# Performance work log

Measured on AMD Instinct MI355X. Metric: run time of the kernel, lower is better.

## Reference

```python
import jax, jax.numpy as jnp
import numpy as np

B, T = 64, 2000
Q_DIM, MEM_DIM, ATT_DIM = 1024, 512, 128
N_FILTERS, KERNEL = 32, 31


def setup_inputs() -> dict:
    key = jax.random.key(0)
    ks = jax.random.split(key, 8)
    s = lambda fan_in: 1.0 / np.sqrt(fan_in)
    return {
        "attention_hidden_state": jax.random.normal(ks[0], (B, Q_DIM), jnp.float32),
        "memory": jax.random.normal(ks[1], (B, T, MEM_DIM), jnp.float32),
        "attention_weights_cat": jax.random.uniform(ks[2], (B, 2, T), jnp.float32),
        "W_query": jax.random.normal(ks[3], (Q_DIM, ATT_DIM), jnp.float32) * s(Q_DIM),
        "W_memory": jax.random.normal(ks[4], (MEM_DIM, ATT_DIM), jnp.float32) * s(MEM_DIM),
        "W_v": jax.random.normal(ks[5], (ATT_DIM, 1), jnp.float32) * s(ATT_DIM),
        "W_conv": jax.random.normal(ks[6], (KERNEL, 2, N_FILTERS), jnp.float32) * s(KERNEL * 2),  # WIO layout
        "W_loc": jax.random.normal(ks[7], (N_FILTERS, ATT_DIM), jnp.float32) * s(N_FILTERS),
    }


def reference(attention_hidden_state, memory, attention_weights_cat,
              W_query, W_memory, W_v, W_conv, W_loc):
    # processed query: [B, 1, D]
    pq = jnp.tanh(attention_hidden_state @ W_query)[:, None, :]
    # processed memory: [B, T, D]
    pm = jnp.tanh(jnp.einsum('btm,md->btd', memory, W_memory))
    # location features: Conv1D 'same', no bias, channels-last input [B, T, 2]
    awc = jnp.transpose(attention_weights_cat, (0, 2, 1))
    conv = jax.lax.conv_general_dilated(
        awc, W_conv, window_strides=(1,), padding='SAME',
        dimension_numbers=('NWC', 'WIO', 'NWC'))  # [B, T, F]
    ploc = jnp.tanh(conv @ W_loc)  # [B, T, D]
    # energies: [B, T]
    energies = jnp.squeeze(jnp.tanh(pq + ploc + pm) @ W_v, -1)
    attention_weights = jax.nn.softmax(energies, axis=1)  # [B, T]
    attention_context = jnp.einsum('bt,btm->bm', attention_weights, memory)
    return attention_context, attention_weights
```

## Files before the change

kernel.cpp:

```cpp
#include <hip/hip_runtime.h>

typedef __attribute__((ext_vector_type(8))) short s16x8;
typedef __attribute__((ext_vector_type(4))) float f32x4;

#define B_SZ 64
#define T_SZ 2000
#define QD 1024
#define MD 512
#define AD 128
#define NF 32
#define KW 31
#define NTILE 63

__device__ __forceinline__ unsigned short f2bf(float f) {
    unsigned int u = __float_as_uint(f);
    unsigned int r = (u + 0x7FFFu + ((u >> 16) & 1u)) >> 16;
    return (unsigned short)r;
}
__device__ __forceinline__ unsigned int pack2bf(float a, float b) {
    return (unsigned int)f2bf(a) | ((unsigned int)f2bf(b) << 16);
}
__device__ __forceinline__ float fast_tanh(float x) {
    float ax = fabsf(x);
    float e = __expf(2.0f * ax);
    float r = 1.0f - 2.0f * __builtin_amdgcn_rcpf(e + 1.0f);
    return x < 0.0f ? -r : r;
}

__global__ __launch_bounds__(256) void prep_kernel(
    const float* __restrict__ ahs, const float* __restrict__ Wq,
    const float* __restrict__ Wm, const float* __restrict__ Wl,
    float* __restrict__ pq, unsigned short* __restrict__ WB,
    unsigned short* __restrict__ WL) {
    const int blk = blockIdx.x, tid = threadIdx.x;
    if (blk < 64) {
        __shared__ float q_sm[QD];
        ((float4*)q_sm)[tid] = ((const float4*)(ahs + blk * QD))[tid];
        __syncthreads();
        if (tid < AD) {
            float acc = 0.0f;
            for (int k = 0; k < QD; ++k) acc += q_sm[k] * Wq[k * AD + tid];
            pq[blk * AD + tid] = fast_tanh(acc);
        }
    } else if (blk < 96) {
        int cidx = (blk - 64) * 256 + tid;
        int n = cidx >> 10, s = (cidx >> 6) & 15, l = cidx & 63;
        int col = n * 16 + (l & 15);
        int krow = s * 32 + (l >> 4) * 8;
        float v[8];
        #pragma unroll
        for (int j = 0; j < 8; ++j) v[j] = Wm[(krow + j) * AD + col];
        uint4 pk;
        pk.x = pack2bf(v[0], v[1]); pk.y = pack2bf(v[2], v[3]);
        pk.z = pack2bf(v[4], v[5]); pk.w = pack2bf(v[6], v[7]);
        *(uint4*)(WB + cidx * 8) = pk;
    } else {
        for (int h = 0; h < 2; ++h) {
            int cidx = h * 256 + tid;
            int n = cidx >> 6, l = cidx & 63;
            int col = n * 16 + (l & 15);
            int krow = (l >> 4) * 8;
            float v[8];
            #pragma unroll
            for (int j = 0; j < 8; ++j) v[j] = Wl[(krow + j) * AD + col];
            uint4 pk;
            pk.x = pack2bf(v[0], v[1]); pk.y = pack2bf(v[2], v[3]);
            pk.z = pack2bf(v[4], v[5]); pk.w = pack2bf(v[6], v[7]);
            *(uint4*)(WL + cidx * 8) = pk;
        }
    }
}

__global__ __launch_bounds__(256) void energy_kernel(
    const float* __restrict__ memory, const float* __restrict__ awcat,
    const float* __restrict__ Wconv, const float* __restrict__ Wv,
    const float* __restrict__ pq, const unsigned short* __restrict__ WB,
    const unsigned short* __restrict__ WL, float* __restrict__ energies,
    float* __restrict__ ctile, float* __restrict__ mloc, int do_fuse) {
    const int tile = blockIdx.x;
    const int b = blockIdx.y;
    const int t0 = tile * 32;
    const int tid = threadIdx.x;

    __shared__ __align__(16) unsigned short Atile[32 * 512];
    __shared__ float aw_sm[2][64];
    __shared__ __align__(16) unsigned short conv_sm[32 * 40];
    __shared__ float e_part[32][4];
    __shared__ float p_sm[32];

    if (tid < 128) {
        int c = tid >> 6, i = tid & 63;
        float v = 0.0f;
        int tv = t0 - 15 + i;
        if (i < 63 && tv >= 0 && tv < T_SZ) v = awcat[(b * 2 + c) * T_SZ + tv];
        aw_sm[c][i] = v;
    }

    {
        const float4* msrc = (const float4*)(memory + ((size_t)b * T_SZ + t0) * MD);
        #pragma unroll
        for (int it = 0; it < 8; ++it) {
            int cid = it * 256 + tid;
            int r = cid >> 6, cc = cid & 63;
            float4 v0 = {0, 0, 0, 0}, v1 = {0, 0, 0, 0};
            if (t0 + r < T_SZ) {
                v0 = msrc[r * 128 + cc * 2];
                v1 = msrc[r * 128 + cc * 2 + 1];
            }
            uint4 pk;
            pk.x = pack2bf(v0.x, v0.y); pk.y = pack2bf(v0.z, v0.w);
            pk.z = pack2bf(v1.x, v1.y); pk.w = pack2bf(v1.z, v1.w);
            int off = (r * 1024 + cc * 16) ^ ((r & 7) << 4);
            *(uint4*)((char*)Atile + off) = pk;
        }
    }
    __syncthreads();

    {
        int f = tid & 31, tq = tid >> 5;
        float acc[4] = {0, 0, 0, 0};
        for (int k = 0; k < KW; ++k) {
            #pragma unroll
            for (int c = 0; c < 2; ++c) {
                float wv = Wconv[(k * 2 + c) * NF + f];
                #pragma unroll
                for (int tt = 0; tt < 4; ++tt)
                    acc[tt] += wv * aw_sm[c][tq + tt * 8 + k];
            }
        }
        #pragma unroll
        for (int tt = 0; tt < 4; ++tt)
            conv_sm[(tq + tt * 8) * 40 + f] = f2bf(acc[tt]);
    }
    __syncthreads();

    const int w = tid >> 6, l = tid & 63;
    const int lr = l & 15, lg = l >> 4;
    const int d0 = (2 * w + 0) * 16 + lr;
    const int d1 = (2 * w + 1) * 16 + lr;
    const float pqv0 = pq[b * AD + d0], pqv1 = pq[b * AD + d1];
    const float wvv0 = Wv[d0], wvv1 = Wv[d1];

    f32x4 zero4 = {0, 0, 0, 0};
    f32x4 p00 = zero4, p01 = zero4, p10 = zero4, p11 = zero4;

    const s16x8* wbp = (const s16x8*)WB;
    const int swz = (lr & 7) << 4;
    const int abase0 = lr * 1024 + lg * 16;
    const int abase1 = (16 + lr) * 1024 + lg * 16;

    #pragma unroll
    for (int s = 0; s < 16; ++s) {
        s16x8 a0 = *(const s16x8*)((const char*)Atile + ((abase0 + s * 64) ^ swz));
        s16x8 a1 = *(const s16x8*)((const char*)Atile + ((abase1 + s * 64) ^ swz));
        s16x8 b0 = wbp[((2 * w + 0) * 16 + s) * 64 + l];
        s16x8 b1 = wbp[((2 * w + 1) * 16 + s) * 64 + l];
        p00 = __builtin_amdgcn_mfma_f32_16x16x32_bf16(a0, b0, p00, 0, 0, 0);
        p01 = __builtin_amdgcn_mfma_f32_16x16x32_bf16(a0, b1, p01, 0, 0, 0);
        p10 = __builtin_amdgcn_mfma_f32_16x16x32_bf16(a1, b0, p10, 0, 0, 0);
        p11 = __builtin_amdgcn_mfma_f32_16x16x32_bf16(a1, b1, p11, 0, 0, 0);
    }

    s16x8 la0 = *(const s16x8*)((const char*)conv_sm + (lr * 80 + lg * 16));
    s16x8 la1 = *(const s16x8*)((const char*)conv_sm + ((16 + lr) * 80 + lg * 16));
    const s16x8* wlp = (const s16x8*)WL;
    s16x8 lb0 = wlp[(2 * w + 0) * 64 + l];
    s16x8 lb1 = wlp[(2 * w + 1) * 64 + l];
    f32x4 q00 = __builtin_amdgcn_mfma_f32_16x16x32_bf16(la0, lb0, zero4, 0, 0, 0);
    f32x4 q01 = __builtin_amdgcn_mfma_f32_16x16x32_bf16(la0, lb1, zero4, 0, 0, 0);
    f32x4 q10 = __builtin_amdgcn_mfma_f32_16x16x32_bf16(la1, lb0, zero4, 0, 0, 0);
    f32x4 q11 = __builtin_amdgcn_mfma_f32_16x16x32_bf16(la1, lb1, zero4, 0, 0, 0);

    float vr[8];
    #pragma unroll
    for (int r = 0; r < 4; ++r) {
        vr[r]     = fast_tanh(pqv0 + fast_tanh(q00[r]) + fast_tanh(p00[r])) * wvv0
                  + fast_tanh(pqv1 + fast_tanh(q01[r]) + fast_tanh(p01[r])) * wvv1;
        vr[4 + r] = fast_tanh(pqv0 + fast_tanh(q10[r]) + fast_tanh(p10[r])) * wvv0
                  + fast_tanh(pqv1 + fast_tanh(q11[r]) + fast_tanh(p11[r])) * wvv1;
    }
    #pragma unroll
    for (int j = 0; j < 8; ++j) {
        float v = vr[j];
        v += __shfl_xor(v, 1);
        v += __shfl_xor(v, 2);
        v += __shfl_xor(v, 4);
        v += __shfl_xor(v, 8);
        if (lr == 0) e_part[(j >> 2) * 16 + lg * 4 + (j & 3)][w] = v;
    }
    __syncthreads();

    if (tid < 32) {
        int t = t0 + tid;
        bool valid = t < T_SZ;
        float e = (e_part[tid][0] + e_part[tid][1]) + (e_part[tid][2] + e_part[tid][3]);
        if (valid) energies[b * T_SZ + t] = e;
        if (do_fuse) {
            float m = valid ? e : -3.4e38f;
            m = fmaxf(m, __shfl_xor(m, 1));
            m = fmaxf(m, __shfl_xor(m, 2));
            m = fmaxf(m, __shfl_xor(m, 4));
            m = fmaxf(m, __shfl_xor(m, 8));
            m = fmaxf(m, __shfl_xor(m, 16));
            p_sm[tid] = valid ? __expf(e - m) : 0.0f;
            if (tid == 0) mloc[b * NTILE + tile] = m;
        }
    }
    if (!do_fuse) return;
    __syncthreads();

    {
        float c0 = 0.0f, c1 = 0.0f;
        const int boff = tid * 4;
        #pragma unroll
        for (int t = 0; t < 32; ++t) {
            float p = p_sm[t];
            unsigned int pk = *(const unsigned int*)(
                (const char*)Atile + ((t * 1024 + boff) ^ ((t & 7) << 4)));
            c0 += p * __uint_as_float(pk << 16);
            c1 += p * __uint_as_float(pk & 0xffff0000u);
        }
        float2 o; o.x = c0; o.y = c1;
        ((float2*)ctile)[((b * NTILE + tile) << 8) + tid] = o;
    }
}

__global__ __launch_bounds__(256) void softmax_kernel(
    const float* __restrict__ energies, float* __restrict__ wout,
    float* __restrict__ Mb, float* __restrict__ invZb) {
    const int b = blockIdx.x, tid = threadIdx.x;
    const int lane = tid & 63, wv = tid >> 6;
    __shared__ float red[8];
    float ev[8];
    float m = -3.4e38f;
    #pragma unroll
    for (int i = 0; i < 8; ++i) {
        int idx = tid + i * 256;
        ev[i] = (idx < T_SZ) ? energies[b * T_SZ + idx] : -3.4e38f;
        m = fmaxf(m, ev[i]);
    }
    m = fmaxf(m, __shfl_xor(m, 1));  m = fmaxf(m, __shfl_xor(m, 2));
    m = fmaxf(m, __shfl_xor(m, 4));  m = fmaxf(m, __shfl_xor(m, 8));
    m = fmaxf(m, __shfl_xor(m, 16)); m = fmaxf(m, __shfl_xor(m, 32));
    if (lane == 0) red[wv] = m;
    __syncthreads();
    m = fmaxf(fmaxf(red[0], red[1]), fmaxf(red[2], red[3]));
    float p[8];
    float s = 0.0f;
    #pragma unroll
    for (int i = 0; i < 8; ++i) {
        int idx = tid + i * 256;
        p[i] = (idx < T_SZ) ? __expf(ev[i] - m) : 0.0f;
        s += p[i];
    }
    s += __shfl_xor(s, 1);  s += __shfl_xor(s, 2);
    s += __shfl_xor(s, 4);  s += __shfl_xor(s, 8);
    s += __shfl_xor(s, 16); s += __shfl_xor(s, 32);
    if (lane == 0) red[4 + wv] = s;
    __syncthreads();
    float Z = (red[4] + red[5]) + (red[6] + red[7]);
    float inv = 1.0f / Z;
    if (tid == 0) { Mb[b] = m; invZb[b] = inv; }
    #pragma unroll
    for (int i = 0; i < 8; ++i) {
        int idx = tid + i * 256;
        if (idx < T_SZ) wout[b * T_SZ + idx] = p[i] * inv;
    }
}

__global__ __launch_bounds__(256) void ctx_reduce_fused_kernel(
    const float* __restrict__ ctile, const float* __restrict__ mloc,
    const float* __restrict__ Mb, const float* __restrict__ invZb,
    float* __restrict__ ctx) {
    const int b = blockIdx.x, tid = threadIdx.x;
    const float M = Mb[b], iZ = invZb[b];
    float2 acc = {0.0f, 0.0f};
    #pragma unroll 7
    for (int tl = 0; tl < NTILE; ++tl) {
        float sc = __expf(mloc[b * NTILE + tl] - M);
        float2 v = ((const float2*)ctile)[((b * NTILE + tl) << 8) + tid];
        acc.x += sc * v.x;
        acc.y += sc * v.y;
    }
    float2 o; o.x = acc.x * iZ; o.y = acc.y * iZ;
    ((float2*)ctx)[(b << 8) + tid] = o;
}

__global__ __launch_bounds__(256) void ctx_partial_kernel(
    const float* __restrict__ memory, const float* __restrict__ wts,
    float* __restrict__ part) {
    const int ci = blockIdx.x, b = blockIdx.y, tid = threadIdx.x;
    const float2* m2 = (const float2*)memory;
    float2 acc = {0.0f, 0.0f};
    const int t0 = ci * 100, t1 = t0 + 100;
    #pragma unroll 4
    for (int t = t0; t < t1; ++t) {
        float wgt = wts[b * T_SZ + t];
        float2 v = m2[((size_t)(b * T_SZ + t)) * 256 + tid];
        acc.x += wgt * v.x;
        acc.y += wgt * v.y;
    }
    ((float2*)part)[(b * 20 + ci) * 256 + tid] = acc;
}

__global__ __launch_bounds__(256) void ctx_reduce_kernel(
    const float* __restrict__ part, float* __restrict__ ctx) {
    const int b = blockIdx.x, tid = threadIdx.x;
    const float2* p2 = (const float2*)part;
    float2 acc = {0.0f, 0.0f};
    #pragma unroll
    for (int ci = 0; ci < 20; ++ci) {
        float2 v = p2[(b * 20 + ci) * 256 + tid];
        acc.x += v.x;
        acc.y += v.y;
    }
    ((float2*)ctx)[b * 256 + tid] = acc;
}

extern "C" void kernel_launch(void* const* d_in, const int* in_sizes, int n_in,
                              void* d_out, int out_size, void* d_ws, size_t ws_size,
                              hipStream_t stream) {
    const float* ahs    = (const float*)d_in[0];
    const float* memory = (const float*)d_in[1];
    const float* awcat  = (const float*)d_in[2];
    const float* Wq     = (const float*)d_in[3];
    const float* Wm     = (const float*)d_in[4];
    const float* Wv     = (const float*)d_in[5];
    const float* Wconv  = (const float*)d_in[6];
    const float* Wl     = (const float*)d_in[7];

    float* out = (float*)d_out;
    float* ctx = out;
    float* wts = out + B_SZ * MD;

    char* ws = (char*)d_ws;
    float* pq             = (float*)(ws);
    unsigned short* WB    = (unsigned short*)(ws + 32768);
    unsigned short* WL    = (unsigned short*)(ws + 163840);
    float* energies       = (float*)(ws + 172032);
    float* mloc           = (float*)(ws + 684032);
    float* Mb             = (float*)(ws + 700416);
    float* invZb          = (float*)(ws + 700672);
    float* ctile          = (float*)(ws + 701440);
    float* part           = (float*)(ws + 701440);

    const size_t need_fused = 701440 + (size_t)B_SZ * NTILE * MD * 4;
    const int do_fuse = (ws_size >= need_fused) ? 1 : 0;

    prep_kernel<<<97, 256, 0, stream>>>(ahs, Wq, Wm, Wl, pq, WB, WL);
    energy_kernel<<<dim3(NTILE, 64), 256, 0, stream>>>(
        memory, awcat, Wconv, Wv, pq, WB, WL, energies, ctile, mloc, do_fuse);
    softmax_kernel<<<64, 256, 0, stream>>>(energies, wts, Mb, invZb);
    if (do_fuse) {
        ctx_reduce_fused_kernel<<<64, 256, 0, stream>>>(ctile, mloc, Mb, invZb, ctx);
    } else {
        ctx_partial_kernel<<<dim3(20, 64), 256, 0, stream>>>(memory, wts, part);
        ctx_reduce_kernel<<<64, 256, 0, stream>>>(part, ctx);
    }
}
```

Measured before the change: 107.0 us.

## Fuse softmax with context reduction, pad LDS tile stride, split query GEMV

Merges the softmax and the tile-context reduction into one kernel, which removes a launch and the round trip through global memory for the per-batch max and normaliser. Pads the shared-memory row stride of the bf16 memory tile from 1024 to 1056 bytes to spread LDS bank accesses. Splits the query projection across all 256 threads with four independent accumulators. Replaces the manual bf16 packing of memory with the HIP intrinsic, which should match round-to-nearest-even but may treat NaN differently.

```diff
diff --git a/kernel.cpp b/kernel.cpp
--- a/kernel.cpp
+++ b/kernel.cpp
@@ -1,4 +1,5 @@
 #include <hip/hip_runtime.h>
+#include <hip/hip_bf16.h>
 
 typedef __attribute__((ext_vector_type(8))) short s16x8;
 typedef __attribute__((ext_vector_type(4))) float f32x4;
@@ -11,14 +12,20 @@
 #define NF 32
 #define KW 31
 #define NTILE 63
+#define ASTRIDE 1056
 
 __device__ __forceinline__ unsigned short f2bf(float f) {
     unsigned int u = __float_as_uint(f);
     unsigned int r = (u + 0x7FFFu + ((u >> 16) & 1u)) >> 16;
     return (unsigned short)r;
 }
+__device__ __forceinline__ unsigned int pack2bf_manual(float a, float b) {
+    return (unsigned int)f2bf(a) | ((unsigned int)f2bf(b) << 16);
+}
 __device__ __forceinline__ unsigned int pack2bf(float a, float b) {
-    return (unsigned int)f2bf(a) | ((unsigned int)f2bf(b) << 16);
+    union { __hip_bfloat162 h; unsigned int u; } cv;
+    cv.h = __float22bfloat162_rn(float2{a, b});
+    return cv.u;
 }
 __device__ __forceinline__ float fast_tanh(float x) {
     float ax = fabsf(x);
@@ -35,13 +42,22 @@
     const int blk = blockIdx.x, tid = threadIdx.x;
     if (blk < 64) {
         __shared__ float q_sm[QD];
+        __shared__ float part[AD];
         ((float4*)q_sm)[tid] = ((const float4*)(ahs + blk * QD))[tid];
         __syncthreads();
-        if (tid < AD) {
-            float acc = 0.0f;
-            for (int k = 0; k < QD; ++k) acc += q_sm[k] * Wq[k * AD + tid];
-            pq[blk * AD + tid] = fast_tanh(acc);
-        }
+        const int d = tid & 127, kh = tid >> 7;
+        const int k0 = kh * 512;
+        float a0 = 0, a1 = 0, a2 = 0, a3 = 0;
+        for (int k = k0; k < k0 + 512; k += 4) {
+            a0 += q_sm[k]     * Wq[(k)     * AD + d];
+            a1 += q_sm[k + 1] * Wq[(k + 1) * AD + d];
+            a2 += q_sm[k + 2] * Wq[(k + 2) * AD + d];
+            a3 += q_sm[k + 3] * Wq[(k + 3) * AD + d];
+        }
+        float s = (a0 + a1) + (a2 + a3);
+        if (kh) part[d] = s;
+        __syncthreads();
+        if (tid < AD) pq[blk * AD + tid] = fast_tanh(s + part[tid]);
     } else if (blk < 96) {
         int cidx = (blk - 64) * 256 + tid;
         int n = cidx >> 10, s = (cidx >> 6) & 15, l = cidx & 63;
@@ -64,8 +80,8 @@
             #pragma unroll
             for (int j = 0; j < 8; ++j) v[j] = Wl[(krow + j) * AD + col];
             uint4 pk;
-            pk.x = pack2bf(v[0], v[1]); pk.y = pack2bf(v[2], v[3]);
-            pk.z = pack2bf(v[4], v[5]); pk.w = pack2bf(v[6], v[7]);
+            pk.x = pack2bf_manual(v[0], v[1]); pk.y = pack2bf_manual(v[2], v[3]);
+            pk.z = pack2bf_manual(v[4], v[5]); pk.w = pack2bf_manual(v[6], v[7]);
             *(uint4*)(WL + cidx * 8) = pk;
         }
     }
@@ -82,7 +98,7 @@
     const int t0 = tile * 32;
     const int tid = threadIdx.x;
 
-    __shared__ __align__(16) unsigned short Atile[32 * 512];
+    __shared__ __align__(16) unsigned short Atile[32 * (ASTRIDE / 2)];
     __shared__ float aw_sm[2][64];
     __shared__ __align__(16) unsigned short conv_sm[32 * 40];
     __shared__ float e_part[32][4];
@@ -110,7 +126,7 @@
             uint4 pk;
             pk.x = pack2bf(v0.x, v0.y); pk.y = pack2bf(v0.z, v0.w);
             pk.z = pack2bf(v1.x, v1.y); pk.w = pack2bf(v1.z, v1.w);
-            int off = (r * 1024 + cc * 16) ^ ((r & 7) << 4);
+            int off = r * ASTRIDE + ((cc * 16) ^ ((r & 7) << 4));
             *(uint4*)((char*)Atile + off) = pk;
         }
     }
@@ -146,13 +162,15 @@
 
     const s16x8* wbp = (const s16x8*)WB;
     const int swz = (lr & 7) << 4;
-    const int abase0 = lr * 1024 + lg * 16;
-    const int abase1 = (16 + lr) * 1024 + lg * 16;
+    const int rbase0 = lr * ASTRIDE;
+    const int rbase1 = (16 + lr) * ASTRIDE;
+    const int inb = lg * 16;
 
     #pragma unroll
     for (int s = 0; s < 16; ++s) {
-        s16x8 a0 = *(const s16x8*)((const char*)Atile + ((abase0 + s * 64) ^ swz));
-        s16x8 a1 = *(const s16x8*)((const char*)Atile + ((abase1 + s * 64) ^ swz));
+        int j = (inb + s * 64) ^ swz;
+        s16x8 a0 = *(const s16x8*)((const char*)Atile + rbase0 + j);
+        s16x8 a1 = *(const s16x8*)((const char*)Atile + rbase1 + j);
         s16x8 b0 = wbp[((2 * w + 0) * 16 + s) * 64 + l];
         s16x8 b1 = wbp[((2 * w + 1) * 16 + s) * 64 + l];
         p00 = __builtin_amdgcn_mfma_f32_16x16x32_bf16(a0, b0, p00, 0, 0, 0);
@@ -216,7 +234,7 @@
         for (int t = 0; t < 32; ++t) {
             float p = p_sm[t];
             unsigned int pk = *(const unsigned int*)(
-                (const char*)Atile + ((t * 1024 + boff) ^ ((t & 7) << 4)));
+                (const char*)Atile + t * ASTRIDE + (boff ^ ((t & 7) << 4)));
             c0 += p * __uint_as_float(pk << 16);
             c1 += p * __uint_as_float(pk & 0xffff0000u);
         }
@@ -225,9 +243,64 @@
     }
 }
 
+__global__ __launch_bounds__(256) void softmax_ctx_kernel(
+    const float* __restrict__ energies, const float* __restrict__ mloc,
+    const float* __restrict__ ctile, float* __restrict__ wout,
+    float* __restrict__ ctx) {
+    const int b = blockIdx.x, tid = threadIdx.x;
+    const int lane = tid & 63, wv = tid >> 6;
+    __shared__ float red[8];
+    __shared__ float sc_sm[NTILE];
+    float ev[8];
+    float m = -3.4e38f;
+    #pragma unroll
+    for (int i = 0; i < 8; ++i) {
+        int idx = tid + i * 256;
+        ev[i] = (idx < T_SZ) ? energies[b * T_SZ + idx] : -3.4e38f;
+        m = fmaxf(m, ev[i]);
+    }
+    m = fmaxf(m, __shfl_xor(m, 1));  m = fmaxf(m, __shfl_xor(m, 2));
+    m = fmaxf(m, __shfl_xor(m, 4));  m = fmaxf(m, __shfl_xor(m, 8));
+    m = fmaxf(m, __shfl_xor(m, 16)); m = fmaxf(m, __shfl_xor(m, 32));
+    if (lane == 0) red[wv] = m;
+    __syncthreads();
+    m = fmaxf(fmaxf(red[0], red[1]), fmaxf(red[2], red[3]));
+    float p[8];
+    float s = 0.0f;
+    #pragma unroll
+    for (int i = 0; i < 8; ++i) {
+        int idx = tid + i * 256;
+        p[i] = (idx < T_SZ) ? __expf(ev[i] - m) : 0.0f;
+        s += p[i];
+    }
+    s += __shfl_xor(s, 1);  s += __shfl_xor(s, 2);
+    s += __shfl_xor(s, 4);  s += __shfl_xor(s, 8);
+    s += __shfl_xor(s, 16); s += __shfl_xor(s, 32);
+    if (lane == 0) red[4 + wv] = s;
+    __syncthreads();
+    float Z = (red[4] + red[5]) + (red[6] + red[7]);
+    float inv = 1.0f / Z;
+    #pragma unroll
+    for (int i = 0; i < 8; ++i) {
+        int idx = tid + i * 256;
+        if (idx < T_SZ) wout[b * T_SZ + idx] = p[i] * inv;
+    }
+    if (tid < NTILE) sc_sm[tid] = __expf(mloc[b * NTILE + tid] - m) * inv;
+    __syncthreads();
+
+    float2 acc = {0.0f, 0.0f};
+    #pragma unroll 7
+    for (int tl = 0; tl < NTILE; ++tl) {
+        float sc = sc_sm[tl];
+        float2 v = ((const float2*)ctile)[((b * NTILE + tl) << 8) + tid];
+        acc.x += sc * v.x;
+        acc.y += sc * v.y;
+    }
+    ((float2*)ctx)[(b << 8) + tid] = acc;
+}
+
 __global__ __launch_bounds__(256) void softmax_kernel(
-    const float* __restrict__ energies, float* __restrict__ wout,
-    float* __restrict__ Mb, float* __restrict__ invZb) {
+    const float* __restrict__ energies, float* __restrict__ wout) {
     const int b = blockIdx.x, tid = threadIdx.x;
     const int lane = tid & 63, wv = tid >> 6;
     __shared__ float red[8];
@@ -260,30 +333,11 @@
     __syncthreads();
     float Z = (red[4] + red[5]) + (red[6] + red[7]);
     float inv = 1.0f / Z;
-    if (tid == 0) { Mb[b] = m; invZb[b] = inv; }
     #pragma unroll
     for (int i = 0; i < 8; ++i) {
         int idx = tid + i * 256;
         if (idx < T_SZ) wout[b * T_SZ + idx] = p[i] * inv;
     }
-}
-
-__global__ __launch_bounds__(256) void ctx_reduce_fused_kernel(
-    const float* __restrict__ ctile, const float* __restrict__ mloc,
-    const float* __restrict__ Mb, const float* __restrict__ invZb,
-    float* __restrict__ ctx) {
-    const int b = blockIdx.x, tid = threadIdx.x;
-    const float M = Mb[b], iZ = invZb[b];
-    float2 acc = {0.0f, 0.0f};
-    #pragma unroll 7
-    for (int tl = 0; tl < NTILE; ++tl) {
-        float sc = __expf(mloc[b * NTILE + tl] - M);
-        float2 v = ((const float2*)ctile)[((b * NTILE + tl) << 8) + tid];
-        acc.x += sc * v.x;
-        acc.y += sc * v.y;
-    }
-    float2 o; o.x = acc.x * iZ; o.y = acc.y * iZ;
-    ((float2*)ctx)[(b << 8) + tid] = o;
 }
 
 __global__ __launch_bounds__(256) void ctx_partial_kernel(
@@ -339,8 +393,6 @@
     unsigned short* WL    = (unsigned short*)(ws + 163840);
     float* energies       = (float*)(ws + 172032);
     float* mloc           = (float*)(ws + 684032);
-    float* Mb             = (float*)(ws + 700416);
-    float* invZb          = (float*)(ws + 700672);
     float* ctile          = (float*)(ws + 701440);
     float* part           = (float*)(ws + 701440);
 
@@ -350,10 +402,10 @@
     prep_kernel<<<97, 256, 0, stream>>>(ahs, Wq, Wm, Wl, pq, WB, WL);
     energy_kernel<<<dim3(NTILE, 64), 256, 0, stream>>>(
         memory, awcat, Wconv, Wv, pq, WB, WL, energies, ctile, mloc, do_fuse);
-    softmax_kernel<<<64, 256, 0, stream>>>(energies, wts, Mb, invZb);
     if (do_fuse) {
-        ctx_reduce_fused_kernel<<<64, 256, 0, stream>>>(ctile, mloc, Mb, invZb, ctx);
+        softmax_ctx_kernel<<<64, 256, 0, stream>>>(energies, mloc, ctile, wts, ctx);
     } else {
+        softmax_kernel<<<64, 256, 0, stream>>>(energies, wts);
         ctx_partial_kernel<<<dim3(20, 64), 256, 0, stream>>>(memory, wts, part);
         ctx_reduce_kernel<<<64, 256, 0, stream>>>(part, ctx);
     }
```

After: 96.67 us. 9.6% less time.
